# Performance work log

Hardware: AMD Instinct MI355X
Metric: run time of the kernel (lower is better)

## Reference

```python
import jax, jax.numpy as jnp
import numpy as np

NV, NQ, K, C, FF, H = 40000, 8192, 96, 128, 256, 8
DH = C // H


def _layernorm(x, g, b, eps=1e-5):
    m = jnp.mean(x, axis=-1, keepdims=True)
    v = jnp.var(x, axis=-1, keepdims=True)
    return (x - m) * jax.lax.rsqrt(v + eps) * g + b


def setup_inputs() -> dict:
    key = jax.random.key(0)
    ks = jax.random.split(key, 20)
    voxel_features = jax.random.normal(ks[0], (NV, C), dtype=jnp.float32)
    voxel_coords = jax.random.normal(ks[1], (NV, 3), dtype=jnp.float32)
    query_coords = jax.random.normal(ks[2], (NQ, 3), dtype=jnp.float32)
    raw = jax.random.randint(ks[3], (NQ, K), 0, 50000)
    key_indices = jnp.where(raw >= NV, -1, raw)  # -1 marks padded/missing keys
    key_indices = key_indices.at[:, 0].set(raw[:, 0] % NV)  # ensure >=1 valid key per query
    w = lambda k, shape: (jax.random.normal(k, shape, dtype=jnp.float32) * 0.02)
    return {
        "voxel_features": voxel_features,
        "voxel_coords": voxel_coords,
        "query_coords": query_coords,
        "key_indices": key_indices,
        "norm1_g": jnp.ones((C,), jnp.float32), "norm1_b": jnp.zeros((C,), jnp.float32),
        "q_pos_w": w(ks[4], (C, 3)), "q_pos_b": jnp.zeros((C,), jnp.float32),
        "k_pos_w": w(ks[5], (C, 3)), "k_pos_b": jnp.zeros((C,), jnp.float32),
        "in_w": w(ks[6], (3 * C, C)), "in_b": jnp.zeros((3 * C,), jnp.float32),
        "out_w": w(ks[7], (C, C)), "out_b": jnp.zeros((C,), jnp.float32),
        "norm2_g": jnp.ones((C,), jnp.float32), "norm2_b": jnp.zeros((C,), jnp.float32),
        "lin1_w": w(ks[8], (FF, C)), "lin1_b": jnp.zeros((FF,), jnp.float32),
        "lin2_w": w(ks[9], (C, FF)), "lin2_b": jnp.zeros((C,), jnp.float32),
        "fin_w": w(ks[10], (C, C)), "fin_b": jnp.zeros((C,), jnp.float32),
    }


def reference(voxel_features, voxel_coords, query_coords, key_indices,
              norm1_g, norm1_b, q_pos_w, q_pos_b, k_pos_w, k_pos_b,
              in_w, in_b, out_w, out_b, norm2_g, norm2_b,
              lin1_w, lin1_b, lin2_w, lin2_b, fin_w, fin_b):
    mask = key_indices < 0                      # [NQ, K] True = padded
    idx = jnp.where(mask, 0, key_indices)
    vf = _layernorm(voxel_features, norm1_g, norm1_b)   # norm1
    key_feat = vf[idx]                          # gather: [NQ, K, C]
    key_c = voxel_coords[idx]                   # [NQ, K, 3]
    # q_pos_proj: Linear(3,C)+ReLU ; k_pos_proj: Conv1d(3,C,1)+ReLU (== per-key linear)
    q_feat = jax.nn.relu(query_coords @ q_pos_w.T + q_pos_b)        # [NQ, C]
    key_pos = jax.nn.relu(jnp.einsum('nkt,ct->nkc', key_c, k_pos_w) + k_pos_b)
    key_feat = key_feat + key_pos               # [NQ, K, C]
    # nn.MultiheadAttention: query [1,NQ,C], key/value [K,NQ,C] -> per-query attention over K keys
    wq, wk, wv = in_w[:C], in_w[C:2 * C], in_w[2 * C:]
    bq, bk, bv = in_b[:C], in_b[C:2 * C], in_b[2 * C:]
    q = (q_feat @ wq.T + bq).reshape(NQ, H, DH)                 # [NQ,H,DH]
    k = (key_feat @ wk.T + bk).reshape(NQ, K, H, DH)            # [NQ,K,H,DH]
    v = (key_feat @ wv.T + bv).reshape(NQ, K, H, DH)
    scale = 1.0 / np.sqrt(DH)
    scores = jnp.einsum('nhd,nkhd->nhk', q, k) * scale          # [NQ,H,K]
    scores = jnp.where(mask[:, None, :], jnp.float32(-1e9), scores)
    attn = jax.nn.softmax(scores, axis=-1)
    ctx = jnp.einsum('nhk,nkhd->nhd', attn, v).reshape(NQ, C)
    attend = ctx @ out_w.T + out_b                              # [NQ,C]
    # FFN block (dropout=0 -> identity)
    h = _layernorm(attend, norm2_g, norm2_b)
    act = jax.nn.relu(h @ lin1_w.T + lin1_b) @ lin2_w.T + lin2_b
    x = attend + act
    out = jax.nn.relu(x @ fin_w.T + fin_b)                      # output_layer
    return out
```

## Files before the change

### kernel.cpp

```cpp
#include <hip/hip_runtime.h>
#include <hip/hip_bf16.h>
#include <math.h>

constexpr int NVOX = 40000;
constexpr int NQRY = 8192;
constexpr int KK   = 96;
constexpr int CH   = 128;
constexpr int FFD  = 256;

typedef __attribute__((ext_vector_type(8))) short short8;
typedef __attribute__((ext_vector_type(4))) float float4v;

__device__ inline float bflo(unsigned u) { return __uint_as_float(u << 16); }
__device__ inline float bfhi(unsigned u) { return __uint_as_float(u & 0xffff0000u); }
__device__ inline unsigned short f2bf(float x) {
  union { float f; unsigned u; } a; a.f = x;
  const unsigned r = a.u + 0x7fffu + ((a.u >> 16) & 1u);
  return (unsigned short)(r >> 16);
}
__device__ inline unsigned pack2(float lo, float hi) {
  return (unsigned)f2bf(lo) | ((unsigned)f2bf(hi) << 16);
}

__global__ __launch_bounds__(256) void k_prep(
    const float* __restrict__ vfeat, const float* __restrict__ vcoord,
    const float* __restrict__ n1g, const float* __restrict__ n1b,
    const float* __restrict__ kpw, const float* __restrict__ kpb,
    const float* __restrict__ in_w,
    const float* __restrict__ ow, const float* __restrict__ l1w,
    const float* __restrict__ l2w, const float* __restrict__ fw,
    __hip_bfloat16* __restrict__ Gb, __hip_bfloat16* __restrict__ Wb,
    __hip_bfloat16* __restrict__ Eb) {
  const int b = blockIdx.x;
  const int t = threadIdx.x;
  if (b < NVOX/16) {
    const int vloc = t >> 4;
    const int l    = t & 15;
    const int j = b * 16 + vloc;
    const float4* vrow = reinterpret_cast<const float4*>(vfeat + (size_t)j * CH);
    const float4 x0 = vrow[l*2], x1 = vrow[l*2+1];
    float s  = x0.x+x0.y+x0.z+x0.w + x1.x+x1.y+x1.z+x1.w;
    float ss = x0.x*x0.x+x0.y*x0.y+x0.z*x0.z+x0.w*x0.w
             + x1.x*x1.x+x1.y*x1.y+x1.z*x1.z+x1.w*x1.w;
    #pragma unroll
    for (int m = 8; m >= 1; m >>= 1) { s += __shfl_xor(s, m); ss += __shfl_xor(ss, m); }
    const float mean = s * (1.0f/CH);
    const float var  = ss * (1.0f/CH) - mean*mean;
    const float rstd = 1.0f / sqrtf(var + 1e-5f);
    const float c0 = vcoord[j*3+0], c1 = vcoord[j*3+1], c2 = vcoord[j*3+2];
    const float xv[8] = {x0.x,x0.y,x0.z,x0.w,x1.x,x1.y,x1.z,x1.w};
    float gv[8];
    #pragma unroll
    for (int u = 0; u < 8; u++) {
      const int c = l*8 + u;
      const float vf = (xv[u] - mean) * rstd * n1g[c] + n1b[c];
      const float kp = fmaf(c0, kpw[c*3+0], fmaf(c1, kpw[c*3+1], fmaf(c2, kpw[c*3+2], kpb[c])));
      gv[u] = vf + fmaxf(kp, 0.0f);
    }
    const uint4 pk = make_uint4(pack2(gv[0],gv[1]), pack2(gv[2],gv[3]),
                                pack2(gv[4],gv[5]), pack2(gv[6],gv[7]));
    *reinterpret_cast<uint4*>(Gb + (size_t)j*CH + l*8) = pk;
  } else {
    const int idx = b - NVOX/16;
    const float* src;
    __hip_bfloat16* dst;
    if (idx < 8) {
      const int e = (idx * 256 + t) * 16;
      src = in_w + (size_t)CH*CH + e;
      dst = Wb + e;
    } else {
      const int f = ((idx - 8) * 256 + t) * 16;
      dst = Eb + f;
      if      (f < 16384) src = ow  + f;
      else if (f < 49152) src = l1w + (f - 16384);
      else if (f < 81920) src = l2w + (f - 49152);
      else                src = fw  + (f - 81920);
    }
    float v[16];
    #pragma unroll
    for (int u = 0; u < 4; u++) {
      const float4 fq = *reinterpret_cast<const float4*>(src + u*4);
      v[u*4+0]=fq.x; v[u*4+1]=fq.y; v[u*4+2]=fq.z; v[u*4+3]=fq.w;
    }
    uint4* o = reinterpret_cast<uint4*>(dst);
    o[0] = make_uint4(pack2(v[0],v[1]), pack2(v[2],v[3]),
                      pack2(v[4],v[5]), pack2(v[6],v[7]));
    o[1] = make_uint4(pack2(v[8],v[9]), pack2(v[10],v[11]),
                      pack2(v[12],v[13]), pack2(v[14],v[15]));
  }
}

__global__ __launch_bounds__(256) void k_kv_gemm(
    const __hip_bfloat16* __restrict__ Gb, const __hip_bfloat16* __restrict__ Wb,
    const float* __restrict__ in_b,
    __hip_bfloat16* __restrict__ Kp, __hip_bfloat16* __restrict__ Vp) {
  __shared__ unsigned short ldsD[64][72];
  const int t = threadIdx.x;
  const int w = t >> 6;
  const int lane = t & 63;
  const int col = lane & 15;
  const int quad = lane >> 4;
  const int bx = blockIdx.x;
  const int v0 = (bx >> 2) * 64;
  const int cg = bx & 3;

  const unsigned short* gRow =
      reinterpret_cast<const unsigned short*>(Gb) + (size_t)(v0 + w*16 + col)*CH + quad*8;
  short8 afrag[4];
  #pragma unroll
  for (int kq = 0; kq < 4; kq++)
    afrag[kq] = *reinterpret_cast<const short8*>(gRow + kq*32);

  float4v acc[4];
  #pragma unroll
  for (int j = 0; j < 4; j++) {
    const float bia = in_b[CH + cg*64 + j*16 + col];
    acc[j] = (float4v){bia, bia, bia, bia};
  }
  const unsigned short* wB = reinterpret_cast<const unsigned short*>(Wb);
  #pragma unroll
  for (int kq = 0; kq < 4; kq++) {
    #pragma unroll
    for (int j = 0; j < 4; j++) {
      const short8 bfrag = *reinterpret_cast<const short8*>(
          wB + (size_t)(cg*64 + j*16 + col)*CH + kq*32 + quad*8);
      acc[j] = __builtin_amdgcn_mfma_f32_16x16x32_bf16(afrag[kq], bfrag, acc[j], 0, 0, 0);
    }
  }
  #pragma unroll
  for (int j = 0; j < 4; j++)
    #pragma unroll
    for (int r = 0; r < 4; r++)
      ldsD[w*16 + quad*4 + r][j*16 + col] = f2bf(acc[j][r]);
  __syncthreads();
  const int row = t >> 2;
  const int cc  = (t & 3) * 16;
  const uint4 d0 = *reinterpret_cast<const uint4*>(&ldsD[row][cc]);
  const uint4 d1 = *reinterpret_cast<const uint4*>(&ldsD[row][cc+8]);
  __hip_bfloat16* dst = (cg < 2) ? Kp : Vp;
  uint4* out = reinterpret_cast<uint4*>(dst + (size_t)(v0 + row)*CH + (cg & 1)*64 + cc);
  out[0] = d0; out[1] = d1;
}

__global__ __launch_bounds__(256) void k_query(
    const float* __restrict__ qcoord,
    const float* __restrict__ qpw, const float* __restrict__ qpb,
    const float* __restrict__ in_w, const float* __restrict__ in_b,
    float* __restrict__ qout) {
  __shared__ float qf[16][CH];
  const int t = threadIdx.x;
  const int qbase = blockIdx.x * 16;
  #pragma unroll
  for (int i = 0; i < 8; i++) {
    const int e = t + 256*i;
    const int qv = e >> 7, c = e & 127;
    const int qq = qbase + qv;
    const float v = fmaf(qcoord[qq*3+0], qpw[c*3+0],
                    fmaf(qcoord[qq*3+1], qpw[c*3+1],
                    fmaf(qcoord[qq*3+2], qpw[c*3+2], qpb[c])));
    qf[qv][c] = fmaxf(v, 0.0f);
  }
  __syncthreads();
  const int oc = t & 127, half = t >> 7;
  const float* wrow = in_w + (size_t)oc * CH;
  const float bia = in_b[oc];
  float acc[8];
  #pragma unroll
  for (int v = 0; v < 8; v++) acc[v] = bia;
  for (int c = 0; c < CH; c += 4) {
    const float4 w4 = *reinterpret_cast<const float4*>(wrow + c);
    #pragma unroll
    for (int v = 0; v < 8; v++) {
      const float4 g4 = *reinterpret_cast<const float4*>(&qf[half*8+v][c]);
      acc[v] = fmaf(g4.x, w4.x, fmaf(g4.y, w4.y, fmaf(g4.z, w4.z, fmaf(g4.w, w4.w, acc[v]))));
    }
  }
  #pragma unroll
  for (int v = 0; v < 8; v++) qout[(size_t)(qbase + half*8 + v)*CH + oc] = acc[v];
}

__global__ __launch_bounds__(256) void k_attn(
    const __hip_bfloat16* __restrict__ Kp, const __hip_bfloat16* __restrict__ Vp,
    const float* __restrict__ qg, const int* __restrict__ kidx,
    float* __restrict__ ctxg) {
  __shared__ float qs[CH];
  __shared__ int   js[KK];
  __shared__ float sc[8*100];
  __shared__ float red[4][CH];
  __shared__ float rden[8];
  const int n = blockIdx.x;
  const int t = threadIdx.x;
  if (t < CH) qs[t] = qg[(size_t)n*CH + t];
  if (t < KK) js[t] = kidx[(size_t)n*KK + t];
  __syncthreads();
  #pragma unroll
  for (int i = 0; i < 3; i++) {
    const int e = t + 256*i;
    const int k = e >> 3, h = e & 7;
    const int j = js[k];
    float s;
    if (j < 0) {
      s = -1e9f;
    } else {
      const uint4* kr = reinterpret_cast<const uint4*>(Kp + (size_t)j*CH + h*16);
      const uint4 ka = kr[0], kb = kr[1];
      const float* qh = qs + h*16;
      s = 0.0f;
      s = fmaf(qh[0],  bflo(ka.x), s); s = fmaf(qh[1],  bfhi(ka.x), s);
      s = fmaf(qh[2],  bflo(ka.y), s); s = fmaf(qh[3],  bfhi(ka.y), s);
      s = fmaf(qh[4],  bflo(ka.z), s); s = fmaf(qh[5],  bfhi(ka.z), s);
      s = fmaf(qh[6],  bflo(ka.w), s); s = fmaf(qh[7],  bfhi(ka.w), s);
      s = fmaf(qh[8],  bflo(kb.x), s); s = fmaf(qh[9],  bfhi(kb.x), s);
      s = fmaf(qh[10], bflo(kb.y), s); s = fmaf(qh[11], bfhi(kb.y), s);
      s = fmaf(qh[12], bflo(kb.z), s); s = fmaf(qh[13], bfhi(kb.z), s);
      s = fmaf(qh[14], bflo(kb.w), s); s = fmaf(qh[15], bfhi(kb.w), s);
      s *= 0.25f;
    }
    sc[h*100 + k] = s;
  }
  __syncthreads();
  if (t < 128) {
    const int h = t >> 4, l = t & 15;
    float mx = -3e38f;
    for (int k = l; k < KK; k += 16) mx = fmaxf(mx, sc[h*100+k]);
    #pragma unroll
    for (int m = 8; m >= 1; m >>= 1) mx = fmaxf(mx, __shfl_xor(mx, m));
    float sum = 0.0f;
    for (int k = l; k < KK; k += 16) {
      const float p = __expf(sc[h*100+k] - mx);
      sc[h*100+k] = p;
      sum += p;
    }
    #pragma unroll
    for (int m = 8; m >= 1; m >>= 1) sum += __shfl_xor(sum, m);
    if (l == 0) rden[h] = 1.0f / sum;
  }
  __syncthreads();
  {
    const int p = t & 63, grp = t >> 6;
    const int h = p >> 3;
    float a0 = 0.0f, a1 = 0.0f;
    const int k0 = grp * 24;
    for (int k = k0; k < k0 + 24; k++) {
      const int j = js[k];
      if (j >= 0) {
        const unsigned vv = reinterpret_cast<const unsigned*>(Vp + (size_t)j*CH)[p];
        const float w = sc[h*100+k];
        a0 = fmaf(w, bflo(vv), a0);
        a1 = fmaf(w, bfhi(vv), a1);
      }
    }
    *reinterpret_cast<float2*>(&red[grp][2*p]) = make_float2(a0, a1);
  }
  __syncthreads();
  if (t < CH) {
    ctxg[(size_t)n*CH + t] =
        (red[0][t] + red[1][t] + red[2][t] + red[3][t]) * rden[t>>4];
  }
}

__global__ __launch_bounds__(256) void k_epi(
    const float* __restrict__ ctxg, const __hip_bfloat16* __restrict__ Eb,
    const float* __restrict__ ob,
    const float* __restrict__ n2g, const float* __restrict__ n2b,
    const float* __restrict__ l1b, const float* __restrict__ l2b,
    const float* __restrict__ fb,
    float* __restrict__ outp) {
  __shared__ unsigned short csb[16][136];
  __shared__ float attnS[16][132];
  __shared__ unsigned short hb[16][136];
  __shared__ unsigned short a1b[16][264];
  __shared__ unsigned short xb[16][136];
  const unsigned short* owb  = reinterpret_cast<const unsigned short*>(Eb);
  const unsigned short* l1wb = owb + 16384;
  const unsigned short* l2wb = owb + 49152;
  const unsigned short* fwb  = owb + 81920;

  const int t = threadIdx.x;
  const int w = t >> 6;
  const int lane = t & 63;
  const int col = lane & 15;
  const int quad = lane >> 4;
  const int qbase = blockIdx.x * 16;

  {
    const int e = t * 8;
    const int row = e >> 7, cc = e & 127;
    const float4* src = reinterpret_cast<const float4*>(ctxg + (size_t)(qbase+row)*CH + cc);
    const float4 x0 = src[0], x1 = src[1];
    *reinterpret_cast<uint4*>(&csb[row][cc]) =
        make_uint4(pack2(x0.x,x0.y), pack2(x0.z,x0.w), pack2(x1.x,x1.y), pack2(x1.z,x1.w));
  }
  __syncthreads();
  {
    short8 af[4];
    #pragma unroll
    for (int kq = 0; kq < 4; kq++)
      af[kq] = *reinterpret_cast<const short8*>(&csb[col][quad*8 + kq*32]);
    #pragma unroll
    for (int j = 0; j < 2; j++) {
      const int n0 = w*32 + j*16;
      const float bia = ob[n0 + col];
      float4v acc = (float4v){bia, bia, bia, bia};
      #pragma unroll
      for (int kq = 0; kq < 4; kq++) {
        const short8 bf = *reinterpret_cast<const short8*>(
            owb + (size_t)(n0 + col)*CH + kq*32 + quad*8);
        acc = __builtin_amdgcn_mfma_f32_16x16x32_bf16(af[kq], bf, acc, 0, 0, 0);
      }
      #pragma unroll
      for (int r = 0; r < 4; r++) attnS[quad*4 + r][n0 + col] = acc[r];
    }
  }
  __syncthreads();
  {
    const int row = t >> 4, l = t & 15;
    float s = 0.0f, ss = 0.0f;
    #pragma unroll
    for (int c = l; c < CH; c += 16) { const float x = attnS[row][c]; s += x; ss += x*x; }
    #pragma unroll
    for (int m = 8; m >= 1; m >>= 1) { s += __shfl_xor(s, m); ss += __shfl_xor(ss, m); }
    const float mean = s * (1.0f/CH);
    const float var  = ss * (1.0f/CH) - mean*mean;
    const float rstd = 1.0f / sqrtf(var + 1e-5f);
    #pragma unroll
    for (int c = l; c < CH; c += 16)
      hb[row][c] = f2bf((attnS[row][c] - mean) * rstd * n2g[c] + n2b[c]);
  }
  __syncthreads();
  {
    short8 af[4];
    #pragma unroll
    for (int kq = 0; kq < 4; kq++)
      af[kq] = *reinterpret_cast<const short8*>(&hb[col][quad*8 + kq*32]);
    #pragma unroll
    for (int j = 0; j < 4; j++) {
      const int n0 = w*64 + j*16;
      const float bia = l1b[n0 + col];
      float4v acc = (float4v){bia, bia, bia, bia};
      #pragma unroll
      for (int kq = 0; kq < 4; kq++) {
        const short8 bf = *reinterpret_cast<const short8*>(
            l1wb + (size_t)(n0 + col)*CH + kq*32 + quad*8);
        acc = __builtin_amdgcn_mfma_f32_16x16x32_bf16(af[kq], bf, acc, 0, 0, 0);
      }
      #pragma unroll
      for (int r = 0; r < 4; r++)
        a1b[quad*4 + r][n0 + col] = f2bf(fmaxf(acc[r], 0.0f));
    }
  }
  __syncthreads();
  {
    short8 af[8];
    #pragma unroll
    for (int kq = 0; kq < 8; kq++)
      af[kq] = *reinterpret_cast<const short8*>(&a1b[col][quad*8 + kq*32]);
    #pragma unroll
    for (int j = 0; j < 2; j++) {
      const int n0 = w*32 + j*16;
      const float bia = l2b[n0 + col];
      float4v acc = (float4v){bia, bia, bia, bia};
      #pragma unroll
      for (int kq = 0; kq < 8; kq++) {
        const short8 bf = *reinterpret_cast<const short8*>(
            l2wb + (size_t)(n0 + col)*FFD + kq*32 + quad*8);
        acc = __builtin_amdgcn_mfma_f32_16x16x32_bf16(af[kq], bf, acc, 0, 0, 0);
      }
      #pragma unroll
      for (int r = 0; r < 4; r++)
        xb[quad*4 + r][n0 + col] = f2bf(acc[r] + attnS[quad*4 + r][n0 + col]);
    }
  }
  __syncthreads();
  {
    short8 af[4];
    #pragma unroll
    for (int kq = 0; kq < 4; kq++)
      af[kq] = *reinterpret_cast<const short8*>(&xb[col][quad*8 + kq*32]);
    #pragma unroll
    for (int j = 0; j < 2; j++) {
      const int n0 = w*32 + j*16;
      const float bia = fb[n0 + col];
      float4v acc = (float4v){bia, bia, bia, bia};
      #pragma unroll
      for (int kq = 0; kq < 4; kq++) {
        const short8 bf = *reinterpret_cast<const short8*>(
            fwb + (size_t)(n0 + col)*CH + kq*32 + quad*8);
        acc = __builtin_amdgcn_mfma_f32_16x16x32_bf16(af[kq], bf, acc, 0, 0, 0);
      }
      #pragma unroll
      for (int r = 0; r < 4; r++)
        outp[(size_t)(qbase + quad*4 + r)*CH + n0 + col] = fmaxf(acc[r], 0.0f);
    }
  }
}

extern "C" void kernel_launch(void* const* d_in, const int* in_sizes, int n_in,
                              void* d_out, int out_size, void* d_ws, size_t ws_size,
                              hipStream_t stream) {
  const float* vfeat  = (const float*)d_in[0];
  const float* vcoord = (const float*)d_in[1];
  const float* qcoord = (const float*)d_in[2];
  const int*   kidx   = (const int*)  d_in[3];
  const float* n1g    = (const float*)d_in[4];
  const float* n1b    = (const float*)d_in[5];
  const float* qpw    = (const float*)d_in[6];
  const float* qpb    = (const float*)d_in[7];
  const float* kpw    = (const float*)d_in[8];
  const float* kpb    = (const float*)d_in[9];
  const float* in_w   = (const float*)d_in[10];
  const float* in_b   = (const float*)d_in[11];
  const float* out_w  = (const float*)d_in[12];
  const float* out_b  = (const float*)d_in[13];
  const float* n2g    = (const float*)d_in[14];
  const float* n2b    = (const float*)d_in[15];
  const float* l1w    = (const float*)d_in[16];
  const float* l1b    = (const float*)d_in[17];
  const float* l2w    = (const float*)d_in[18];
  const float* l2b    = (const float*)d_in[19];
  const float* fw     = (const float*)d_in[20];
  const float* fb     = (const float*)d_in[21];
  float* out = (float*)d_out;

  __hip_bfloat16* Kp = (__hip_bfloat16*)d_ws;
  __hip_bfloat16* Vp = Kp + (size_t)NVOX*CH;
  __hip_bfloat16* Gb = Vp + (size_t)NVOX*CH;
  __hip_bfloat16* Wb = Gb + (size_t)NVOX*CH;
  __hip_bfloat16* Eb = Wb + (size_t)2*CH*CH;
  float* qb = (float*)(Eb + 98304);
  float* cx = qb + (size_t)NQRY*CH;

  k_prep   <<<NVOX/16 + 32, 256, 0, stream>>>(vfeat, vcoord, n1g, n1b, kpw, kpb,
                                              in_w, out_w, l1w, l2w, fw, Gb, Wb, Eb);
  k_query  <<<NQRY/16, 256, 0, stream>>>(qcoord, qpw, qpb, in_w, in_b, qb);
  k_kv_gemm<<<(NVOX/64)*4, 256, 0, stream>>>(Gb, Wb, in_b, Kp, Vp);
  k_attn   <<<NQRY,    256, 0, stream>>>(Kp, Vp, qb, kidx, cx);
  k_epi    <<<NQRY/16, 256, 0, stream>>>(cx, Eb, out_b, n2g, n2b, l1b, l2b, fb, out);
}
```

Baseline: 219.5 us.

## Store K/V head-major interleaved and split attention blocks per head

The K/V projection output is rewritten into a head-major layout in which each voxel's 16 K values and 16 V values for one head sit together in a 64-byte record. The attention kernel now gives each block 8 queries times one head instead of one query times all heads, so each block reads only one head's slab. The goal is better L2/cache locality, since each head's working set is an eighth of the K/V data, and one record fetch serves both the K and V access for a head. In exchange, each block reloads the key indices for its 8 queries, and the V loads become narrower 4-byte strided accesses within the record.

```diff
diff --git a/kernel.cpp b/kernel.cpp
--- a/kernel.cpp
+++ b/kernel.cpp
@@ -93,7 +93,7 @@
 __global__ __launch_bounds__(256) void k_kv_gemm(
     const __hip_bfloat16* __restrict__ Gb, const __hip_bfloat16* __restrict__ Wb,
     const float* __restrict__ in_b,
-    __hip_bfloat16* __restrict__ Kp, __hip_bfloat16* __restrict__ Vp) {
+    unsigned short* __restrict__ KVh) {
   __shared__ unsigned short ldsD[64][72];
   const int t = threadIdx.x;
   const int w = t >> 6;
@@ -137,8 +137,10 @@
   const int cc  = (t & 3) * 16;
   const uint4 d0 = *reinterpret_cast<const uint4*>(&ldsD[row][cc]);
   const uint4 d1 = *reinterpret_cast<const uint4*>(&ldsD[row][cc+8]);
-  __hip_bfloat16* dst = (cg < 2) ? Kp : Vp;
-  uint4* out = reinterpret_cast<uint4*>(dst + (size_t)(v0 + row)*CH + (cg & 1)*64 + cc);
+  const int head = (cg & 1) * 4 + (cc >> 4);
+  const int isV  = cg >> 1;
+  unsigned short* dst = KVh + ((size_t)head*NVOX + (v0 + row))*32 + isV*16;
+  uint4* out = reinterpret_cast<uint4*>(dst);
   out[0] = d0; out[1] = d1;
 }
 
@@ -180,31 +182,39 @@
 }
 
 __global__ __launch_bounds__(256) void k_attn(
-    const __hip_bfloat16* __restrict__ Kp, const __hip_bfloat16* __restrict__ Vp,
+    const unsigned short* __restrict__ KVh,
     const float* __restrict__ qg, const int* __restrict__ kidx,
     float* __restrict__ ctxg) {
-  __shared__ float qs[CH];
-  __shared__ int   js[KK];
-  __shared__ float sc[8*100];
-  __shared__ float red[4][CH];
+  __shared__ float qs[8][16];
+  __shared__ int   js[8*KK];
+  __shared__ float sc[8*KK];
+  __shared__ float red[4][8][16];
   __shared__ float rden[8];
-  const int n = blockIdx.x;
-  const int t = threadIdx.x;
-  if (t < CH) qs[t] = qg[(size_t)n*CH + t];
-  if (t < KK) js[t] = kidx[(size_t)n*KK + t];
+  const int t  = threadIdx.x;
+  const int h  = blockIdx.x & 7;
+  const int n0 = (blockIdx.x >> 3) * 8;
+  const unsigned short* KVbase = KVh + (size_t)h * NVOX * 32;
+
+  #pragma unroll
+  for (int i = 0; i < 3; i++)
+    js[t + 256*i] = kidx[(size_t)n0*KK + t + 256*i];
+  if (t < 128) {
+    const int q = t >> 4, d = t & 15;
+    qs[q][d] = qg[(size_t)(n0 + q)*CH + h*16 + d];
+  }
   __syncthreads();
   #pragma unroll
   for (int i = 0; i < 3; i++) {
     const int e = t + 256*i;
-    const int k = e >> 3, h = e & 7;
-    const int j = js[k];
+    const int q = e / KK, k = e - q*KK;
+    const int j = js[e];
     float s;
     if (j < 0) {
       s = -1e9f;
     } else {
-      const uint4* kr = reinterpret_cast<const uint4*>(Kp + (size_t)j*CH + h*16);
+      const uint4* kr = reinterpret_cast<const uint4*>(KVbase + (size_t)j*32);
       const uint4 ka = kr[0], kb = kr[1];
-      const float* qh = qs + h*16;
+      const float* qh = qs[q];
       s = 0.0f;
       s = fmaf(qh[0],  bflo(ka.x), s); s = fmaf(qh[1],  bfhi(ka.x), s);
       s = fmaf(qh[2],  bflo(ka.y), s); s = fmaf(qh[3],  bfhi(ka.y), s);
@@ -216,46 +226,47 @@
       s = fmaf(qh[14], bflo(kb.w), s); s = fmaf(qh[15], bfhi(kb.w), s);
       s *= 0.25f;
     }
-    sc[h*100 + k] = s;
+    sc[e] = s;
   }
   __syncthreads();
   if (t < 128) {
-    const int h = t >> 4, l = t & 15;
+    const int q = t >> 4, l = t & 15;
     float mx = -3e38f;
-    for (int k = l; k < KK; k += 16) mx = fmaxf(mx, sc[h*100+k]);
+    for (int k = l; k < KK; k += 16) mx = fmaxf(mx, sc[q*KK + k]);
     #pragma unroll
     for (int m = 8; m >= 1; m >>= 1) mx = fmaxf(mx, __shfl_xor(mx, m));
     float sum = 0.0f;
     for (int k = l; k < KK; k += 16) {
-      const float p = __expf(sc[h*100+k] - mx);
-      sc[h*100+k] = p;
+      const float p = __expf(sc[q*KK + k] - mx);
+      sc[q*KK + k] = p;
       sum += p;
     }
     #pragma unroll
     for (int m = 8; m >= 1; m >>= 1) sum += __shfl_xor(sum, m);
-    if (l == 0) rden[h] = 1.0f / sum;
-  }
-  __syncthreads();
-  {
-    const int p = t & 63, grp = t >> 6;
-    const int h = p >> 3;
+    if (l == 0) rden[q] = 1.0f / sum;
+  }
+  __syncthreads();
+  {
+    const int q = t >> 5, cp = (t >> 2) & 7, kg = t & 3;
     float a0 = 0.0f, a1 = 0.0f;
-    const int k0 = grp * 24;
+    const int k0 = kg * 24;
     for (int k = k0; k < k0 + 24; k++) {
-      const int j = js[k];
+      const int j = js[q*KK + k];
       if (j >= 0) {
-        const unsigned vv = reinterpret_cast<const unsigned*>(Vp + (size_t)j*CH)[p];
-        const float w = sc[h*100+k];
+        const unsigned vv = *reinterpret_cast<const unsigned*>(
+            KVbase + (size_t)j*32 + 16 + cp*2);
+        const float w = sc[q*KK + k];
         a0 = fmaf(w, bflo(vv), a0);
         a1 = fmaf(w, bfhi(vv), a1);
       }
     }
-    *reinterpret_cast<float2*>(&red[grp][2*p]) = make_float2(a0, a1);
-  }
-  __syncthreads();
-  if (t < CH) {
-    ctxg[(size_t)n*CH + t] =
-        (red[0][t] + red[1][t] + red[2][t] + red[3][t]) * rden[t>>4];
+    *reinterpret_cast<float2*>(&red[kg][q][cp*2]) = make_float2(a0, a1);
+  }
+  __syncthreads();
+  if (t < 128) {
+    const int q = t >> 4, d = t & 15;
+    ctxg[(size_t)(n0 + q)*CH + h*16 + d] =
+        (red[0][q][d] + red[1][q][d] + red[2][q][d] + red[3][q][d]) * rden[q];
   }
 }
 
@@ -422,9 +433,8 @@
   const float* fb     = (const float*)d_in[21];
   float* out = (float*)d_out;
 
-  __hip_bfloat16* Kp = (__hip_bfloat16*)d_ws;
-  __hip_bfloat16* Vp = Kp + (size_t)NVOX*CH;
-  __hip_bfloat16* Gb = Vp + (size_t)NVOX*CH;
+  unsigned short* KVh = (unsigned short*)d_ws;
+  __hip_bfloat16* Gb = (__hip_bfloat16*)(KVh + (size_t)8*NVOX*32);
   __hip_bfloat16* Wb = Gb + (size_t)NVOX*CH;
   __hip_bfloat16* Eb = Wb + (size_t)2*CH*CH;
   float* qb = (float*)(Eb + 98304);
@@ -433,7 +443,7 @@
   k_prep   <<<NVOX/16 + 32, 256, 0, stream>>>(vfeat, vcoord, n1g, n1b, kpw, kpb,
                                               in_w, out_w, l1w, l2w, fw, Gb, Wb, Eb);
   k_query  <<<NQRY/16, 256, 0, stream>>>(qcoord, qpw, qpb, in_w, in_b, qb);
-  k_kv_gemm<<<(NVOX/64)*4, 256, 0, stream>>>(Gb, Wb, in_b, Kp, Vp);
-  k_attn   <<<NQRY,    256, 0, stream>>>(Kp, Vp, qb, kidx, cx);
+  k_kv_gemm<<<(NVOX/64)*4, 256, 0, stream>>>(Gb, Wb, in_b, KVh);
+  k_attn   <<<(NQRY/8)*8, 256, 0, stream>>>(KVh, qb, kidx, cx);
   k_epi    <<<NQRY/16, 256, 0, stream>>>(cx, Eb, out_b, n2g, n2b, l1b, l2b, fb, out);
 }
```

New measurement: 226.6 us. 1.03x slower.
